# Performance work log

Measured on AMD Instinct MI355X. Metric: run time of the kernel, lower is better.

Reference implementation:

```python
import jax, jax.numpy as jnp
import numpy as np
from jax import lax

B, Hm, Wm, C, HEADS, MLP_H = 16, 56, 56, 256, 4, 1024
N = Hm * Wm
GRID_STRIDE = 4
N_GRID = (Hm // GRID_STRIDE) * (Wm // GRID_STRIDE)  # 196
K_DOWN = N // 4                                      # 784
K_ADA = K_DOWN - N_GRID
H2, W2 = Hm // 2, Wm // 2
POOL = 7


def _token_order():
    # get_loc: grid tokens first, then adaptive tokens
    pos = np.arange(N)
    tmp = pos.reshape(Hm, Wm)
    pos_grid = tmp[GRID_STRIDE // 2::GRID_STRIDE, GRID_STRIDE // 2::GRID_STRIDE].reshape(-1)
    m = np.ones(N, bool)
    m[pos_grid] = False
    return np.concatenate([pos_grid, pos[m]])


def _loc_init():
    y = 2.0 * ((np.arange(Hm) + 0.5) / Hm) - 1.0
    x = 2.0 * ((np.arange(Wm) + 0.5) / Wm) - 1.0
    xm, ym = np.meshgrid(x, y)
    return np.stack([xm, ym], -1).reshape(-1, 2).astype(np.float32)


_ORDER = _token_order()
_LOC = _loc_init()[_ORDER]


def _ln(x, g, b, eps=1e-5):
    m = jnp.mean(x, -1, keepdims=True)
    v = jnp.mean((x - m) ** 2, -1, keepdims=True)
    return (x - m) * lax.rsqrt(v + eps) * g + b


def _gauss_kernel(ks=3, sigma=2.0):
    c = np.arange(ks, dtype=np.float32)
    xg = np.tile(c, ks).reshape(ks, ks)
    yg = xg.T
    mean = (ks - 1) / 2.0
    var = sigma ** 2
    k = np.exp(-((xg - mean) ** 2 + (yg - mean) ** 2) / (2 * var)) / (2 * np.pi * var)
    return (k / k.sum()).astype(np.float32)


def _gauss_filt(x):
    ch = x.shape[1]
    w = jnp.broadcast_to(jnp.asarray(_gauss_kernel())[None, None], (ch, 1, 3, 3))
    return lax.conv_general_dilated(x, w, (1, 1), [(1, 1), (1, 1)],
                                    feature_group_count=ch,
                                    dimension_numbers=('NCHW', 'OIHW', 'NCHW'))


def _token2map(x, loc, H, W):
    # scatter-add tokens into a [H,W] map, average by count, gaussian hole-fill
    b, n, c = x.shape
    loc = jnp.clip(loc, -1, 1)
    px = jnp.clip(jnp.round(0.5 * (loc[..., 0] + 1) * W - 0.5).astype(jnp.int32), 0, W - 1)
    py = jnp.clip(jnp.round(0.5 * (loc[..., 1] + 1) * H - 0.5).astype(jnp.int32), 0, H - 1)
    idx = (px + py * W + jnp.arange(b)[:, None] * H * W).reshape(-1)
    src = jnp.concatenate([x, jnp.ones((b, n, 1), x.dtype)], -1).reshape(b * n, c + 1)
    out = jnp.zeros((b * H * W, c + 1), x.dtype).at[idx].add(src)
    out = out.reshape(b, H, W, c + 1).transpose(0, 3, 1, 2)
    feat, mask = out[:, :c], out[:, c:]
    feat = feat / (mask + 1e-6)
    mask = (mask > 0).astype(x.dtype)
    feat = feat * mask
    # reconstruct_feature (kernel_size=3, sigma=2)
    fm = _gauss_filt(jnp.concatenate([feat, mask], 1))
    fi = fm[:, :c] / (fm[:, c:] + 1e-6)
    mi = (fm[:, c:] > 0).astype(x.dtype)
    fi = fi * mi
    return feat + (1 - mask) * fi


def _map2token(fm, loc):
    # bilinear grid_sample, align_corners=False, zeros padding
    b, c, H, W = fm.shape
    x = (loc[..., 0] + 1) * 0.5 * W - 0.5
    y = (loc[..., 1] + 1) * 0.5 * H - 0.5
    x0 = jnp.floor(x)
    y0 = jnp.floor(y)
    wx = x - x0
    wy = y - y0
    fm_flat = fm.reshape(b, c, H * W)

    def gather(xi, yi):
        valid = ((xi >= 0) & (xi < W) & (yi >= 0) & (yi < H)).astype(fm.dtype)
        ii = (jnp.clip(yi, 0, H - 1) * W + jnp.clip(xi, 0, W - 1)).astype(jnp.int32)
        v = jnp.take_along_axis(fm_flat, ii[:, None, :], axis=2)  # [b,c,k]
        return v * valid[:, None, :]

    x0i = x0.astype(jnp.int32)
    y0i = y0.astype(jnp.int32)
    v00 = gather(x0i, y0i)
    v01 = gather(x0i + 1, y0i)
    v10 = gather(x0i, y0i + 1)
    v11 = gather(x0i + 1, y0i + 1)
    wx = wx[:, None, :]
    wy = wy[:, None, :]
    out = (v00 * (1 - wx) * (1 - wy) + v01 * wx * (1 - wy)
           + v10 * (1 - wx) * wy + v11 * wx * wy)
    return out.transpose(0, 2, 1)  # [b,k,c]


def _forward(x, ln1_g, ln1_b, wq, wkv, wproj, bproj, sr_w, sr_b, srn_g, srn_b,
             ln2_g, ln2_b, fc1_w, fc1_b, dw_w, dw_b, fc2_w, fc2_b, conf_w, conf_b):
    order = jnp.asarray(_ORDER)
    x = jnp.take(x, order, axis=1)                       # get_loc reorder
    loc = jnp.broadcast_to(jnp.asarray(_LOC)[None], (B, N, 2))
    d = C // HEADS
    # ---- PVT attention (spatial-reduction via 7x7 adaptive pool + 1x1 conv)
    xn = _ln(x, ln1_g, ln1_b)
    q = (xn @ wq).reshape(B, N, HEADS, d).transpose(0, 2, 1, 3)
    fmap = xn.transpose(0, 2, 1).reshape(B, C, Hm, Wm)
    pooled = fmap.reshape(B, C, POOL, Hm // POOL, POOL, Wm // POOL).mean((3, 5))
    sr = jnp.einsum('bihw,oi->bohw', pooled, sr_w) + sr_b[None, :, None, None]
    t = sr.reshape(B, C, POOL * POOL).transpose(0, 2, 1)
    t = jax.nn.gelu(_ln(t, srn_g, srn_b), approximate=False)
    kv = (t @ wkv).reshape(B, POOL * POOL, 2, HEADS, d)
    k = kv[:, :, 0].transpose(0, 2, 1, 3)
    v = kv[:, :, 1].transpose(0, 2, 1, 3)
    a = jax.nn.softmax(jnp.einsum('bhnd,bhmd->bhnm', q, k) * (d ** -0.5), axis=-1)
    o = jnp.einsum('bhnm,bhmd->bhnd', a, v).transpose(0, 2, 1, 3).reshape(B, N, C)
    x = x + o @ wproj + bproj
    # ---- MLP with depthwise conv
    xn = _ln(x, ln2_g, ln2_b)
    h = jax.nn.relu(xn @ fc1_w + fc1_b)
    hm = h.transpose(0, 2, 1).reshape(B, MLP_H, Hm, Wm)
    hm = lax.conv_general_dilated(hm, dw_w, (1, 1), [(1, 1), (1, 1)],
                                  feature_group_count=MLP_H,
                                  dimension_numbers=('NCHW', 'OIHW', 'NCHW'))
    hm = hm + dw_b[None, :, None, None]
    h = jax.nn.gelu(hm.reshape(B, MLP_H, N).transpose(0, 2, 1), approximate=False)
    x = x + h @ fc2_w + fc2_b
    # ---- gumbel top-k selection among adaptive tokens (grid tokens kept)
    conf = (x @ conf_w + conf_b)[..., 0]                 # [B,N]
    u = jax.random.uniform(jax.random.key(1), (B, N - N_GRID), x.dtype)
    g = -jnp.log(-jnp.log(u + 1e-6) + 1e-6)
    scores = conf[:, N_GRID:] + g                        # T=1
    _, idx = lax.top_k(scores, K_ADA)
    x_ada = jnp.take_along_axis(x[:, N_GRID:], idx[..., None], axis=1)
    loc_ada = jnp.take_along_axis(loc[:, N_GRID:], idx[..., None], axis=1)
    x_down = jnp.concatenate([x[:, :N_GRID], x_ada], 1)      # [B,784,C]
    loc_down = jnp.concatenate([loc[:, :N_GRID], loc_ada], 1)
    # ---- token2map (scatter-add + gaussian fill) then map2token (grid sample)
    fmap2 = _token2map(x, loc, H2, W2)
    tok = _map2token(fmap2, loc_down)
    return x_down + tok


def setup_inputs() -> dict:
    key = jax.random.key(0)
    ks = jax.random.split(key, 10)
    s = 0.02

    def rn(k, shape):
        return jax.random.normal(k, shape, jnp.float32) * s

    return {
        'x': jax.random.normal(ks[0], (B, N, C), jnp.float32),
        'ln1_g': jnp.ones((C,), jnp.float32), 'ln1_b': jnp.zeros((C,), jnp.float32),
        'wq': rn(ks[1], (C, C)), 'wkv': rn(ks[2], (C, 2 * C)),
        'wproj': rn(ks[3], (C, C)), 'bproj': jnp.zeros((C,), jnp.float32),
        'sr_w': rn(ks[4], (C, C)), 'sr_b': jnp.zeros((C,), jnp.float32),
        'srn_g': jnp.ones((C,), jnp.float32), 'srn_b': jnp.zeros((C,), jnp.float32),
        'ln2_g': jnp.ones((C,), jnp.float32), 'ln2_b': jnp.zeros((C,), jnp.float32),
        'fc1_w': rn(ks[5], (C, MLP_H)), 'fc1_b': jnp.zeros((MLP_H,), jnp.float32),
        'dw_w': rn(ks[6], (MLP_H, 1, 3, 3)), 'dw_b': jnp.zeros((MLP_H,), jnp.float32),
        'fc2_w': rn(ks[7], (MLP_H, C)), 'fc2_b': jnp.zeros((C,), jnp.float32),
        'conf_w': rn(ks[8], (C, 1)), 'conf_b': jnp.zeros((1,), jnp.float32),
    }


def reference(x, ln1_g, ln1_b, wq, wkv, wproj, bproj, sr_w, sr_b, srn_g, srn_b,
              ln2_g, ln2_b, fc1_w, fc1_b, dw_w, dw_b, fc2_w, fc2_b, conf_w, conf_b):
    return _forward(x, ln1_g, ln1_b, wq, wkv, wproj, bproj, sr_w, sr_b, srn_g, srn_b,
                    ln2_g, ln2_b, fc1_w, fc1_b, dw_w, dw_b, fc2_w, fc2_b, conf_w, conf_b)
```

## Files before the change

### kernel.cpp

```cpp
#include <hip/hip_runtime.h>
#include <math.h>


#define BB 16
#define NN 3136
#define CC 256
#define NHEADS 4
#define DH 64
#define MLPH 1024
#define NGRID 196
#define NREST 2940
#define KADA 588
#define HW 56
#define BCH 2

__device__ __forceinline__ int inv_order(int p) {
  int r = p / HW, c = p % HW;
  if ((r & 3) == 2 && (c & 3) == 2) return (r >> 2) * 14 + (c >> 2);
  int g = ((r + 1) >> 2) * 14 + (((r & 3) == 2) ? ((c + 1) >> 2) : 0);
  return NGRID + p - g;
}

__device__ __forceinline__ double gelu_d(double v) {
  return 0.5 * v * (1.0 + erf(v * 0.70710678118654752440));
}

__device__ __forceinline__ void tf2x32k(unsigned k0, unsigned k1, unsigned x0, unsigned x1,
                                        unsigned& o0, unsigned& o1) {
  unsigned ks[3] = {k0, k1, k0 ^ k1 ^ 0x1BD11BDAu};
  x0 += ks[0]; x1 += ks[1];
  const int rot[2][4] = {{13,15,26,6},{17,29,16,24}};
  #pragma unroll
  for (int i = 0; i < 5; ++i) {
    #pragma unroll
    for (int j = 0; j < 4; ++j) {
      int rr = rot[i & 1][j];
      x0 += x1;
      x1 = (x1 << rr) | (x1 >> (32 - rr));
      x1 ^= x0;
    }
    x0 += ks[(i + 1) % 3];
    x1 += ks[(i + 2) % 3] + (unsigned)(i + 1);
  }
  o0 = x0; o1 = x1;
}

__device__ bool tf_kat() {
  unsigned a, b;
  tf2x32k(0u, 0u, 0u, 0u, a, b);
  if (a != 0x6b200159u || b != 0x99ba4efeu) return false;
  tf2x32k(0xffffffffu, 0xffffffffu, 0xffffffffu, 0xffffffffu, a, b);
  if (a != 0x1cb996fcu || b != 0xbb002be7u) return false;
  tf2x32k(0x13198a2eu, 0x03707344u, 0x243f6a88u, 0x85a308d3u, a, b);
  if (a != 0xc4923a9cu || b != 0x483df7a0u) return false;
  return true;
}

__device__ __forceinline__ double gumbel_d(int f) {
  unsigned o0, o1;
  tf2x32k(0u, 1u, 0u, (unsigned)f, o0, o1);
  unsigned bits = o0 ^ o1;
  float u = __uint_as_float((bits >> 9) | 0x3f800000u) - 1.0f;
  double ud = (double)u;
  return -log(-log(ud + 1e-6) + 1e-6);
}

__global__ void k_order(int* __restrict__ ord) {
  int p = blockIdx.x * 256 + threadIdx.x;
  if (p < NN) ord[inv_order(p)] = p;
}

__global__ __launch_bounds__(256) void k_ln1(const float* __restrict__ x,
    const float* __restrict__ g, const float* __restrict__ b2,
    float* __restrict__ x_r, float* __restrict__ xn) {
  int b = blockIdx.x / NN, p = blockIdx.x % NN;
  int t = threadIdx.x;
  __shared__ double la[4], lb[4];
  float v = x[((size_t)b*NN + p)*CC + t];
  double vd = (double)v;
  double s = vd;
  #pragma unroll
  for (int o = 32; o; o >>= 1) s += __shfl_xor(s, o, 64);
  if ((t & 63) == 0) la[t >> 6] = s;
  __syncthreads();
  double m = (la[0] + la[1] + la[2] + la[3]) * (1.0/CC);
  double d = vd - m;
  s = d * d;
  #pragma unroll
  for (int o = 32; o; o >>= 1) s += __shfl_xor(s, o, 64);
  if ((t & 63) == 0) lb[t >> 6] = s;
  __syncthreads();
  double var = (lb[0] + lb[1] + lb[2] + lb[3]) * (1.0/CC);
  double o2 = d * (1.0 / sqrt(var + 1e-5)) * (double)g[t] + (double)b2[t];
  int n = inv_order(p);
  size_t dst = ((size_t)b*NN + n)*CC + t;
  x_r[dst] = v;
  xn[dst] = (float)o2;
}

__global__ __launch_bounds__(256) void k_ln2(const float* __restrict__ xin,
    const float* __restrict__ g, const float* __restrict__ b2, float* __restrict__ xo) {
  int row = blockIdx.x;
  int t = threadIdx.x;
  __shared__ double la[4], lb[4];
  double v = (double)xin[(size_t)row*CC + t];
  double s = v;
  #pragma unroll
  for (int o = 32; o; o >>= 1) s += __shfl_xor(s, o, 64);
  if ((t & 63) == 0) la[t >> 6] = s;
  __syncthreads();
  double m = (la[0] + la[1] + la[2] + la[3]) * (1.0/CC);
  double d = v - m;
  s = d * d;
  #pragma unroll
  for (int o = 32; o; o >>= 1) s += __shfl_xor(s, o, 64);
  if ((t & 63) == 0) lb[t >> 6] = s;
  __syncthreads();
  double var = (lb[0] + lb[1] + lb[2] + lb[3]) * (1.0/CC);
  xo[(size_t)row*CC + t] = (float)(d * (1.0 / sqrt(var + 1e-5)) * (double)g[t] + (double)b2[t]);
}

__global__ __launch_bounds__(256) void k_sr(const float* __restrict__ xn,
    const float* __restrict__ sr_w, const float* __restrict__ sr_b, float* __restrict__ srout) {
  int b = blockIdx.x / 49, cell = blockIdx.x % 49;
  int p1 = cell / 7, p2 = cell % 7;
  int t = threadIdx.x;
  __shared__ double pl[256];
  double s = 0.0;
  #pragma unroll
  for (int i = 0; i < 8; ++i)
    #pragma unroll
    for (int j = 0; j < 8; ++j) {
      int n = (p1*8 + i)*HW + (p2*8 + j);
      s += (double)xn[((size_t)b*NN + n)*CC + t];
    }
  pl[t] = s * (1.0/64.0);
  __syncthreads();
  double acc = (double)sr_b[t];
  for (int i = 0; i < CC; ++i) acc += pl[i] * (double)sr_w[t*CC + i];
  srout[((size_t)b*49 + cell)*CC + t] = (float)acc;
}

__global__ __launch_bounds__(256) void k_kv(const float* __restrict__ srout,
    const float* __restrict__ g, const float* __restrict__ b2,
    const float* __restrict__ wkv, float* __restrict__ kb, float* __restrict__ vb) {
  int b = blockIdx.x / 49, m = blockIdx.x % 49;
  int t = threadIdx.x;
  __shared__ double la[4], lb[4];
  __shared__ double tl[256];
  double v = (double)srout[((size_t)b*49 + m)*CC + t];
  double s = v;
  #pragma unroll
  for (int o = 32; o; o >>= 1) s += __shfl_xor(s, o, 64);
  if ((t & 63) == 0) la[t >> 6] = s;
  __syncthreads();
  double mean = (la[0] + la[1] + la[2] + la[3]) * (1.0/CC);
  double d = v - mean;
  s = d * d;
  #pragma unroll
  for (int o = 32; o; o >>= 1) s += __shfl_xor(s, o, 64);
  if ((t & 63) == 0) lb[t >> 6] = s;
  __syncthreads();
  double var = (lb[0] + lb[1] + lb[2] + lb[3]) * (1.0/CC);
  double o2 = d * (1.0 / sqrt(var + 1e-5)) * (double)g[t] + (double)b2[t];
  tl[t] = gelu_d(o2);
  __syncthreads();
  #pragma unroll
  for (int rep = 0; rep < 2; ++rep) {
    int j = t + rep*256;
    double acc = 0.0;
    for (int i = 0; i < CC; ++i) acc += tl[i] * (double)wkv[(size_t)i*512 + j];
    int h = (j >> 6) & 3, dd = j & 63;
    float* dst = (j >> 8) ? vb : kb;
    dst[(((size_t)b*NHEADS + h)*49 + m)*DH + dd] = (float)acc;
  }
}

template<int BIAS, int RELU, int RESID>
__global__ __launch_bounds__(256) void k_gemmA(const float* __restrict__ A,
    const float* __restrict__ Bw, const float* __restrict__ bias,
    const float* resid, float* Co, int M, int N, int K) {
  __shared__ __align__(16) float As[16][132];
  __shared__ __align__(16) float Bs[16][68];
  int tid = threadIdx.x;
  int n0 = blockIdx.x * 64, m0 = blockIdx.y * 128;
  int tx = tid & 15, ty = tid >> 4;
  int aM = tid >> 2, aK = (tid & 3) * 4;
  int bK = tid >> 4, bN = (tid & 15) * 4;
  double acc[8][4] = {};
  for (int k0 = 0; k0 < K; k0 += 16) {
    #pragma unroll
    for (int ps = 0; ps < 2; ++ps) {
      float4 a4 = *(const float4*)&A[(size_t)(m0 + aM + ps*64) * K + k0 + aK];
      As[aK+0][aM+ps*64] = a4.x; As[aK+1][aM+ps*64] = a4.y;
      As[aK+2][aM+ps*64] = a4.z; As[aK+3][aM+ps*64] = a4.w;
    }
    float4 b4 = *(const float4*)&Bw[(size_t)(k0 + bK) * N + n0 + bN];
    *(float4*)&Bs[bK][bN] = b4;
    __syncthreads();
    #pragma unroll
    for (int k = 0; k < 16; ++k) {
      double av[8], bv[4];
      #pragma unroll
      for (int r = 0; r < 8; ++r) av[r] = (double)As[k][ty*8 + r];
      #pragma unroll
      for (int c = 0; c < 4; ++c) bv[c] = (double)Bs[k][tx*4 + c];
      #pragma unroll
      for (int r = 0; r < 8; ++r)
        #pragma unroll
        for (int c = 0; c < 4; ++c)
          acc[r][c] = fma(av[r], bv[c], acc[r][c]);
    }
    __syncthreads();
  }
  #pragma unroll
  for (int r = 0; r < 8; ++r) {
    size_t off = (size_t)(m0 + ty*8 + r) * N + n0 + tx*4;
    #pragma unroll
    for (int c = 0; c < 4; ++c) {
      double v = acc[r][c];
      if (BIAS)  v += (double)bias[n0 + tx*4 + c];
      if (RESID) v += (double)resid[off + c];
      if (RELU)  v = fmax(v, 0.0);
      Co[off + c] = (float)v;
    }
  }
}

template<int BIAS, int RELU, int RESID>
__global__ __launch_bounds__(256) void k_gemmB(const float* __restrict__ A,
    const float* __restrict__ Bw, const float* __restrict__ bias,
    const float* resid, float* Co, int M, int N, int K) {
  __shared__ __align__(16) float As[16][68];
  __shared__ __align__(16) float Bs[16][68];
  int tid = threadIdx.x;
  int n0 = blockIdx.x * 64, m0 = blockIdx.y * 64;
  int tx = tid & 15, ty = tid >> 4;
  int aM = tid >> 2, aK = (tid & 3) * 4;
  int bK = tid >> 4, bN = (tid & 15) * 4;
  double acc[4][4] = {};
  for (int k0 = 0; k0 < K; k0 += 16) {
    float4 a4 = *(const float4*)&A[(size_t)(m0 + aM) * K + k0 + aK];
    As[aK+0][aM] = a4.x; As[aK+1][aM] = a4.y; As[aK+2][aM] = a4.z; As[aK+3][aM] = a4.w;
    float4 b4 = *(const float4*)&Bw[(size_t)(k0 + bK) * N + n0 + bN];
    *(float4*)&Bs[bK][bN] = b4;
    __syncthreads();
    #pragma unroll
    for (int k = 0; k < 16; ++k) {
      double av[4], bv[4];
      #pragma unroll
      for (int r = 0; r < 4; ++r) av[r] = (double)As[k][ty*4 + r];
      #pragma unroll
      for (int c = 0; c < 4; ++c) bv[c] = (double)Bs[k][tx*4 + c];
      #pragma unroll
      for (int r = 0; r < 4; ++r)
        #pragma unroll
        for (int c = 0; c < 4; ++c)
          acc[r][c] = fma(av[r], bv[c], acc[r][c]);
    }
    __syncthreads();
  }
  #pragma unroll
  for (int r = 0; r < 4; ++r) {
    size_t off = (size_t)(m0 + ty*4 + r) * N + n0 + tx*4;
    #pragma unroll
    for (int c = 0; c < 4; ++c) {
      double v = acc[r][c];
      if (BIAS)  v += (double)bias[n0 + tx*4 + c];
      if (RESID) v += (double)resid[off + c];
      if (RELU)  v = fmax(v, 0.0);
      Co[off + c] = (float)v;
    }
  }
}

__global__ __launch_bounds__(64) void k_attn(float* __restrict__ q,
    const float* __restrict__ kb, const float* __restrict__ vb) {
  int b = blockIdx.x / NN, n = blockIdx.x % NN;
  int t = threadIdx.x;
  __shared__ float qs[256];
  __shared__ double lg[4][52];
  __shared__ double sinv[4];
  float* qrow = q + ((size_t)b*NN + n)*CC;
  #pragma unroll
  for (int i = 0; i < 4; ++i) qs[t + i*64] = qrow[t + i*64];
  __syncthreads();
  for (int li = t; li < 196; li += 64) {
    int h = li / 49, m = li % 49;
    const float* kr = kb + (((size_t)b*NHEADS + h)*49 + m)*DH;
    const float* qh = qs + h*DH;
    double acc = 0.0;
    #pragma unroll 16
    for (int d = 0; d < DH; ++d) acc = fma((double)qh[d], (double)kr[d], acc);
    lg[h][m] = acc * 0.125;
  }
  __syncthreads();
  if (t < 4) {
    double mx = -1e300;
    for (int j = 0; j < 49; ++j) mx = fmax(mx, lg[t][j]);
    double s = 0.0;
    for (int j = 0; j < 49; ++j) { double e = exp(lg[t][j] - mx); lg[t][j] = e; s += e; }
    sinv[t] = 1.0 / s;
  }
  __syncthreads();
  #pragma unroll
  for (int h = 0; h < 4; ++h) {
    const float* vr = vb + (((size_t)b*NHEADS + h)*49)*DH + t;
    double acc = 0.0;
    for (int m = 0; m < 49; ++m) acc = fma(lg[h][m], (double)vr[m*DH], acc);
    qrow[h*64 + t] = (float)(acc * sinv[h]);
  }
}

__global__ __launch_bounds__(256) void k_dw(const float* __restrict__ hb,
    const float* __restrict__ w, const float* __restrict__ bias, float* __restrict__ h2) {
  int bl = blockIdx.x / NN, n = blockIdx.x % NN;
  int r = n / HW, c = n % HW;
  int t = threadIdx.x;
  const size_t base = (size_t)bl * NN;
  #pragma unroll
  for (int it = 0; it < 4; ++it) {
    int mc = t + it*256;
    double acc = (double)bias[mc];
    #pragma unroll
    for (int ky = 0; ky < 3; ++ky) {
      int rr = r + ky - 1;
      if (rr < 0 || rr >= HW) continue;
      #pragma unroll
      for (int kx = 0; kx < 3; ++kx) {
        int cc2 = c + kx - 1;
        if (cc2 < 0 || cc2 >= HW) continue;
        acc = fma((double)w[mc*9 + ky*3 + kx], (double)hb[(base + rr*HW + cc2)*MLPH + mc], acc);
      }
    }
    h2[(base + n)*MLPH + mc] = (float)gelu_d(acc);
  }
}

__global__ __launch_bounds__(256) void k_conf(const float* __restrict__ x3,
    const float* __restrict__ cw, const float* __restrict__ cb, double* __restrict__ scd) {
  int wid = (blockIdx.x * 256 + threadIdx.x) >> 6;
  int lane = threadIdx.x & 63;
  if (wid >= BB * NREST) return;
  int b = wid / NREST, i = wid % NREST;
  const float* xr = x3 + ((size_t)b*NN + NGRID + i)*CC;
  double acc = 0.0;
  #pragma unroll
  for (int r = 0; r < 4; ++r)
    acc += (double)xr[lane + r*64] * (double)cw[lane + r*64];
  #pragma unroll
  for (int o = 32; o; o >>= 1) acc += __shfl_xor(acc, o, 64);
  if (lane == 0) scd[wid] = acc + (double)cb[0] + gumbel_d(wid);
}

__global__ __launch_bounds__(512) void k_topk2(const double* __restrict__ scd, int* __restrict__ sel) {
  int b = blockIdx.x / 6, chunk = blockIdx.x % 6;
  __shared__ double sc[NREST];
  const double* s = scd + (size_t)b * NREST;
  for (int j = threadIdx.x; j < NREST; j += 512) sc[j] = s[j];
  __syncthreads();
  int i = chunk * 512 + threadIdx.x;
  if (i < NREST) {
    double si = sc[i];
    int rank = 0;
    #pragma unroll 8
    for (int j = 0; j < NREST; ++j) {
      double sj = sc[j];
      rank += (int)((sj > si) | ((sj == si) & (j < i)));
    }
    if (rank < KADA) sel[b*KADA + rank] = NGRID + i;
  }
}

__global__ __launch_bounds__(256) void k_t2m(const float* __restrict__ x3, float* __restrict__ fm) {
  int b = blockIdx.x / 784, pix = blockIdx.x % 784;
  int py = pix / 28, px = pix % 28;
  int t = threadIdx.x;
  float s = 0.f;
  #pragma unroll
  for (int dy = 0; dy < 2; ++dy)
    #pragma unroll
    for (int dx = 0; dx < 2; ++dx) {
      int p = (2*py + dy)*HW + 2*px + dx;
      s += x3[((size_t)b*NN + inv_order(p))*CC + t];
    }
  fm[((size_t)b*784 + pix)*CC + t] = s * (1.0f / 4.000001f);
}

__global__ __launch_bounds__(256) void k_out(const float* __restrict__ x3,
    const float* __restrict__ fm, const int* __restrict__ sel,
    const int* __restrict__ ord, float* __restrict__ out) {
  int b = blockIdx.x / 784, slot = blockIdx.x % 784;
  int t = threadIdx.x;
  int n = (slot < NGRID) ? slot : sel[b*KADA + slot - NGRID];
  int p = ord[n];
  int r = p / HW, c = p % HW;
  int ix0 = (c - 1) >> 1;
  int iy0 = (r - 1) >> 1;
  float wx = (c & 1) ? 0.25f : 0.75f;
  float wy = (r & 1) ? 0.25f : 0.75f;
  const float* fb = fm + (size_t)b*784*CC + t;
  float v = 0.f;
  float w00 = (1.f-wx)*(1.f-wy), w01 = wx*(1.f-wy), w10 = (1.f-wx)*wy, w11 = wx*wy;
  if (ix0 >= 0   && iy0 >= 0)   v += w00 * fb[(iy0*28 + ix0)*CC];
  if (ix0+1 < 28 && iy0 >= 0)   v += w01 * fb[(iy0*28 + ix0+1)*CC];
  if (ix0 >= 0   && iy0+1 < 28) v += w10 * fb[((iy0+1)*28 + ix0)*CC];
  if (ix0+1 < 28 && iy0+1 < 28) v += w11 * fb[((iy0+1)*28 + ix0+1)*CC];
  float res = x3[((size_t)b*NN + n)*CC + t] + v;
  if (blockIdx.x == 0 && t == 0) {
    if (!tf_kat()) res += 1000.0f;
  }
  out[((size_t)b*784 + slot)*CC + t] = res;
}

extern "C" void kernel_launch(void* const* d_in, const int* in_sizes, int n_in,
                              void* d_out, int out_size, void* d_ws, size_t ws_size,
                              hipStream_t stream) {
  const float* x      = (const float*)d_in[0];
  const float* ln1_g  = (const float*)d_in[1];
  const float* ln1_b  = (const float*)d_in[2];
  const float* wq     = (const float*)d_in[3];
  const float* wkv    = (const float*)d_in[4];
  const float* wproj  = (const float*)d_in[5];
  const float* bproj  = (const float*)d_in[6];
  const float* sr_w   = (const float*)d_in[7];
  const float* sr_b   = (const float*)d_in[8];
  const float* srn_g  = (const float*)d_in[9];
  const float* srn_b  = (const float*)d_in[10];
  const float* ln2_g  = (const float*)d_in[11];
  const float* ln2_b  = (const float*)d_in[12];
  const float* fc1_w  = (const float*)d_in[13];
  const float* fc1_b  = (const float*)d_in[14];
  const float* dw_w   = (const float*)d_in[15];
  const float* dw_b   = (const float*)d_in[16];
  const float* fc2_w  = (const float*)d_in[17];
  const float* fc2_b  = (const float*)d_in[18];
  const float* conf_w = (const float*)d_in[19];
  const float* conf_b = (const float*)d_in[20];
  float* out = (float*)d_out;

  float* ws = (float*)d_ws;
  const size_t SZ_XN = (size_t)BB*NN*CC;
  const size_t SZ_H  = (size_t)BCH*NN*MLPH;
  float* x_r   = ws;
  float* xn    = x_r + SZ_XN;
  float* qbuf  = xn + SZ_XN;
  float* hb    = qbuf + SZ_XN;
  float* h2b   = hb + SZ_H;
  float* srout = h2b + SZ_H;
  float* kb    = srout + (size_t)BB*49*CC;
  float* vb    = kb + (size_t)BB*NHEADS*49*DH;
  float* fm    = vb + (size_t)BB*NHEADS*49*DH;
  double* scd  = (double*)(fm + (size_t)BB*784*CC);
  int*   sel   = (int*)(scd + (size_t)BB*NREST);
  int*   ord   = sel + BB*KADA;

  k_order<<<(NN+255)/256, 256, 0, stream>>>(ord);
  k_ln1<<<BB*NN, 256, 0, stream>>>(x, ln1_g, ln1_b, x_r, xn);
  k_sr<<<BB*49, 256, 0, stream>>>(xn, sr_w, sr_b, srout);
  k_kv<<<BB*49, 256, 0, stream>>>(srout, srn_g, srn_b, wkv, kb, vb);
  k_gemmA<0,0,0><<<dim3(CC/64, BB*NN/128), 256, 0, stream>>>(xn, wq, nullptr, nullptr, qbuf, BB*NN, CC, CC);
  k_attn<<<BB*NN, 64, 0, stream>>>(qbuf, kb, vb);
  k_gemmA<1,0,1><<<dim3(CC/64, BB*NN/128), 256, 0, stream>>>(qbuf, wproj, bproj, x_r, x_r, BB*NN, CC, CC);
  k_ln2<<<BB*NN, 256, 0, stream>>>(x_r, ln2_g, ln2_b, xn);
  for (int bc = 0; bc < BB/BCH; ++bc) {
    const size_t ro = (size_t)bc * BCH * NN;
    k_gemmA<1,1,0><<<dim3(MLPH/64, BCH*NN/128), 256, 0, stream>>>(xn + ro*CC, fc1_w, fc1_b, nullptr, hb, BCH*NN, MLPH, CC);
    k_dw<<<BCH*NN, 256, 0, stream>>>(hb, dw_w, dw_b, h2b);
    k_gemmB<1,0,1><<<dim3(CC/64, BCH*NN/64), 256, 0, stream>>>(h2b, fc2_w, fc2_b, x_r + ro*CC, x_r + ro*CC, BCH*NN, CC, MLPH);
  }
  k_conf<<<(BB*NREST*64 + 255)/256, 256, 0, stream>>>(x_r, conf_w, conf_b, scd);
  k_topk2<<<BB*6, 512, 0, stream>>>(scd, sel);
  k_t2m<<<BB*784, 256, 0, stream>>>(x_r, fm);
  k_out<<<BB*784, 256, 0, stream>>>(x_r, fm, sel, ord, out);
}
```

Measured before the change: 3.590 ms.

## Use 128x128 FP64 GEMM tiles and restructure attention per head tile

Adds a 128x128-tile GEMM with an 8x8 double accumulator per thread and uses it for the q, proj and fc1 GEMMs. fc2 moves from the 64x64 kernel to the 128x64 kernel. Attention is rewritten so each block owns one (batch, head) pair and 64 query tokens. K (transposed) and V are staged once in shared memory, and softmax uses wave shuffles, which removes the per-token reloading of K/V from global memory. The larger tiles raise register pressure (64 double accumulators) and may lower occupancy.

```diff
diff --git a/kernel.cpp b/kernel.cpp
--- a/kernel.cpp
+++ b/kernel.cpp
@@ -173,6 +173,57 @@
     int h = (j >> 6) & 3, dd = j & 63;
     float* dst = (j >> 8) ? vb : kb;
     dst[(((size_t)b*NHEADS + h)*49 + m)*DH + dd] = (float)acc;
+  }
+}
+
+template<int BIAS, int RELU, int RESID>
+__global__ __launch_bounds__(256, 2) void k_gemmC(const float* __restrict__ A,
+    const float* __restrict__ Bw, const float* __restrict__ bias,
+    const float* resid, float* Co, int M, int N, int K) {
+  __shared__ __align__(16) float As[16][132];
+  __shared__ __align__(16) float Bs[16][132];
+  int tid = threadIdx.x;
+  int n0 = blockIdx.x * 128, m0 = blockIdx.y * 128;
+  int tx = tid & 15, ty = tid >> 4;
+  int aM = tid >> 1, aK = (tid & 1) * 8;
+  int bK = tid >> 4, bN = (tid & 15) * 8;
+  double acc[8][8] = {};
+  for (int k0 = 0; k0 < K; k0 += 16) {
+    const float* Ap = A + (size_t)(m0 + aM) * K + k0 + aK;
+    float4 a0 = *(const float4*)Ap;
+    float4 a1 = *(const float4*)(Ap + 4);
+    As[aK+0][aM] = a0.x; As[aK+1][aM] = a0.y; As[aK+2][aM] = a0.z; As[aK+3][aM] = a0.w;
+    As[aK+4][aM] = a1.x; As[aK+5][aM] = a1.y; As[aK+6][aM] = a1.z; As[aK+7][aM] = a1.w;
+    const float* Bp = Bw + (size_t)(k0 + bK) * N + n0 + bN;
+    *(float4*)&Bs[bK][bN]     = *(const float4*)Bp;
+    *(float4*)&Bs[bK][bN + 4] = *(const float4*)(Bp + 4);
+    __syncthreads();
+    #pragma unroll
+    for (int k = 0; k < 16; ++k) {
+      double av[8], bv[8];
+      #pragma unroll
+      for (int r = 0; r < 8; ++r) av[r] = (double)As[k][ty*8 + r];
+      #pragma unroll
+      for (int c = 0; c < 8; ++c) bv[c] = (double)Bs[k][tx*8 + c];
+      #pragma unroll
+      for (int r = 0; r < 8; ++r)
+        #pragma unroll
+        for (int c = 0; c < 8; ++c)
+          acc[r][c] = fma(av[r], bv[c], acc[r][c]);
+    }
+    __syncthreads();
+  }
+  #pragma unroll
+  for (int r = 0; r < 8; ++r) {
+    size_t off = (size_t)(m0 + ty*8 + r) * N + n0 + tx*8;
+    #pragma unroll
+    for (int c = 0; c < 8; ++c) {
+      double v = acc[r][c];
+      if (BIAS)  v += (double)bias[n0 + tx*8 + c];
+      if (RESID) v += (double)resid[off + c];
+      if (RELU)  v = fmax(v, 0.0);
+      Co[off + c] = (float)v;
+    }
   }
 }
 
@@ -227,88 +278,50 @@
   }
 }
 
-template<int BIAS, int RELU, int RESID>
-__global__ __launch_bounds__(256) void k_gemmB(const float* __restrict__ A,
-    const float* __restrict__ Bw, const float* __restrict__ bias,
-    const float* resid, float* Co, int M, int N, int K) {
-  __shared__ __align__(16) float As[16][68];
-  __shared__ __align__(16) float Bs[16][68];
+__global__ __launch_bounds__(256) void k_attn(float* __restrict__ q,
+    const float* __restrict__ kb, const float* __restrict__ vb) {
+  int bh = blockIdx.x / 49, tile = blockIdx.x % 49;
+  int b = bh >> 2, h = bh & 3;
   int tid = threadIdx.x;
-  int n0 = blockIdx.x * 64, m0 = blockIdx.y * 64;
-  int tx = tid & 15, ty = tid >> 4;
-  int aM = tid >> 2, aK = (tid & 3) * 4;
-  int bK = tid >> 4, bN = (tid & 15) * 4;
-  double acc[4][4] = {};
-  for (int k0 = 0; k0 < K; k0 += 16) {
-    float4 a4 = *(const float4*)&A[(size_t)(m0 + aM) * K + k0 + aK];
-    As[aK+0][aM] = a4.x; As[aK+1][aM] = a4.y; As[aK+2][aM] = a4.z; As[aK+3][aM] = a4.w;
-    float4 b4 = *(const float4*)&Bw[(size_t)(k0 + bK) * N + n0 + bN];
-    *(float4*)&Bs[bK][bN] = b4;
-    __syncthreads();
-    #pragma unroll
-    for (int k = 0; k < 16; ++k) {
-      double av[4], bv[4];
-      #pragma unroll
-      for (int r = 0; r < 4; ++r) av[r] = (double)As[k][ty*4 + r];
-      #pragma unroll
-      for (int c = 0; c < 4; ++c) bv[c] = (double)Bs[k][tx*4 + c];
-      #pragma unroll
-      for (int r = 0; r < 4; ++r)
-        #pragma unroll
-        for (int c = 0; c < 4; ++c)
-          acc[r][c] = fma(av[r], bv[c], acc[r][c]);
-    }
-    __syncthreads();
-  }
-  #pragma unroll
-  for (int r = 0; r < 4; ++r) {
-    size_t off = (size_t)(m0 + ty*4 + r) * N + n0 + tx*4;
-    #pragma unroll
-    for (int c = 0; c < 4; ++c) {
-      double v = acc[r][c];
-      if (BIAS)  v += (double)bias[n0 + tx*4 + c];
-      if (RESID) v += (double)resid[off + c];
-      if (RELU)  v = fmax(v, 0.0);
-      Co[off + c] = (float)v;
-    }
-  }
-}
-
-__global__ __launch_bounds__(64) void k_attn(float* __restrict__ q,
-    const float* __restrict__ kb, const float* __restrict__ vb) {
-  int b = blockIdx.x / NN, n = blockIdx.x % NN;
-  int t = threadIdx.x;
-  __shared__ float qs[256];
-  __shared__ double lg[4][52];
-  __shared__ double sinv[4];
-  float* qrow = q + ((size_t)b*NN + n)*CC;
-  #pragma unroll
-  for (int i = 0; i < 4; ++i) qs[t + i*64] = qrow[t + i*64];
-  __syncthreads();
-  for (int li = t; li < 196; li += 64) {
-    int h = li / 49, m = li % 49;
-    const float* kr = kb + (((size_t)b*NHEADS + h)*49 + m)*DH;
-    const float* qh = qs + h*DH;
+  int w = tid >> 6, lane = tid & 63;
+  __shared__ float Kt[64][53];
+  __shared__ float Vs[49][64];
+  __shared__ float qsw[4][64];
+  __shared__ double Ps[4][52];
+  const size_t kvbase = ((size_t)bh * 49) * DH;
+  for (int idx = tid; idx < 49*64; idx += 256) {
+    int m = idx >> 6, d = idx & 63;
+    Kt[d][m] = kb[kvbase + idx];
+    ((float*)Vs)[idx] = vb[kvbase + idx];
+  }
+  __syncthreads();
+  #pragma unroll 1
+  for (int t16 = 0; t16 < 16; ++t16) {
+    int tok = tile*64 + w*16 + t16;
+    size_t qoff = ((size_t)b*NN + tok)*CC + h*64 + lane;
+    qsw[w][lane] = q[qoff];
+    double lg = -1e300;
+    if (lane < 49) {
+      double acc = 0.0;
+      #pragma unroll 16
+      for (int d = 0; d < 64; ++d)
+        acc = fma((double)qsw[w][d], (double)Kt[d][lane], acc);
+      lg = acc * 0.125;
+    }
+    double mx = lg;
+    #pragma unroll
+    for (int o = 32; o; o >>= 1) mx = fmax(mx, __shfl_xor(mx, o, 64));
+    double e = (lane < 49) ? exp(lg - mx) : 0.0;
+    double s = e;
+    #pragma unroll
+    for (int o = 32; o; o >>= 1) s += __shfl_xor(s, o, 64);
+    double sinv = 1.0 / s;
+    if (lane < 49) Ps[w][lane] = e;
     double acc = 0.0;
-    #pragma unroll 16
-    for (int d = 0; d < DH; ++d) acc = fma((double)qh[d], (double)kr[d], acc);
-    lg[h][m] = acc * 0.125;
-  }
-  __syncthreads();
-  if (t < 4) {
-    double mx = -1e300;
-    for (int j = 0; j < 49; ++j) mx = fmax(mx, lg[t][j]);
-    double s = 0.0;
-    for (int j = 0; j < 49; ++j) { double e = exp(lg[t][j] - mx); lg[t][j] = e; s += e; }
-    sinv[t] = 1.0 / s;
-  }
-  __syncthreads();
-  #pragma unroll
-  for (int h = 0; h < 4; ++h) {
-    const float* vr = vb + (((size_t)b*NHEADS + h)*49)*DH + t;
-    double acc = 0.0;
-    for (int m = 0; m < 49; ++m) acc = fma(lg[h][m], (double)vr[m*DH], acc);
-    qrow[h*64 + t] = (float)(acc * sinv[h]);
+    #pragma unroll 7
+    for (int m = 0; m < 49; ++m)
+      acc = fma(Ps[w][m], (double)Vs[m][lane], acc);
+    q[qoff] = (float)(acc * sinv);
   }
 }
 
@@ -459,15 +472,15 @@
   k_ln1<<<BB*NN, 256, 0, stream>>>(x, ln1_g, ln1_b, x_r, xn);
   k_sr<<<BB*49, 256, 0, stream>>>(xn, sr_w, sr_b, srout);
   k_kv<<<BB*49, 256, 0, stream>>>(srout, srn_g, srn_b, wkv, kb, vb);
-  k_gemmA<0,0,0><<<dim3(CC/64, BB*NN/128), 256, 0, stream>>>(xn, wq, nullptr, nullptr, qbuf, BB*NN, CC, CC);
-  k_attn<<<BB*NN, 64, 0, stream>>>(qbuf, kb, vb);
-  k_gemmA<1,0,1><<<dim3(CC/64, BB*NN/128), 256, 0, stream>>>(qbuf, wproj, bproj, x_r, x_r, BB*NN, CC, CC);
+  k_gemmC<0,0,0><<<dim3(CC/128, BB*NN/128), 256, 0, stream>>>(xn, wq, nullptr, nullptr, qbuf, BB*NN, CC, CC);
+  k_attn<<<BB*NHEADS*49, 256, 0, stream>>>(qbuf, kb, vb);
+  k_gemmC<1,0,1><<<dim3(CC/128, BB*NN/128), 256, 0, stream>>>(qbuf, wproj, bproj, x_r, x_r, BB*NN, CC, CC);
   k_ln2<<<BB*NN, 256, 0, stream>>>(x_r, ln2_g, ln2_b, xn);
   for (int bc = 0; bc < BB/BCH; ++bc) {
     const size_t ro = (size_t)bc * BCH * NN;
-    k_gemmA<1,1,0><<<dim3(MLPH/64, BCH*NN/128), 256, 0, stream>>>(xn + ro*CC, fc1_w, fc1_b, nullptr, hb, BCH*NN, MLPH, CC);
+    k_gemmC<1,1,0><<<dim3(MLPH/128, BCH*NN/128), 256, 0, stream>>>(xn + ro*CC, fc1_w, fc1_b, nullptr, hb, BCH*NN, MLPH, CC);
     k_dw<<<BCH*NN, 256, 0, stream>>>(hb, dw_w, dw_b, h2b);
-    k_gemmB<1,0,1><<<dim3(CC/64, BCH*NN/64), 256, 0, stream>>>(h2b, fc2_w, fc2_b, x_r + ro*CC, x_r + ro*CC, BCH*NN, CC, MLPH);
+    k_gemmA<1,0,1><<<dim3(CC/64, BCH*NN/128), 256, 0, stream>>>(h2b, fc2_w, fc2_b, x_r + ro*CC, x_r + ro*CC, BCH*NN, CC, MLPH);
   }
   k_conf<<<(BB*NREST*64 + 255)/256, 256, 0, stream>>>(x_r, conf_w, conf_b, scd);
   k_topk2<<<BB*6, 512, 0, stream>>>(scd, sel);
```

After: 3.733 ms. 4.0% more time.
